# Performance work log

Hardware: AMD Instinct MI355X
Metric: run time of the kernel (lower is better)

Reference implementation:

```python
import jax, jax.numpy as jnp
import numpy as np

DIM = 128
WH, WW = 8, 8
N = WH * WW            # tokens per window = 64
H = 8                  # num_heads
HD = DIM // H          # head_dim = 16
SCALE = HD ** -0.5
B = 2                  # true batch
NW = 1024              # windows per image (256x256 / 8x8)
B_ = B * NW            # 2048 windows total
NFT = 2                # num_frame_type
TABLE = (2 * WH - 1) * (2 * WW - 1)  # 225


def _relative_position_index():
    coords = np.stack(np.meshgrid(np.arange(WH), np.arange(WW), indexing='ij'))  # (2, WH, WW)
    cf = coords.reshape(2, -1)                        # (2, N)
    rel = cf[:, :, None] - cf[:, None, :]             # (2, N, N)
    rel = rel.transpose(1, 2, 0).astype(np.int64)     # (N, N, 2)
    rel[..., 0] += WH - 1
    rel[..., 1] += WW - 1
    rel[..., 0] *= 2 * WW - 1
    return rel.sum(-1)                                # (N, N) in [0, 224]


def setup_inputs() -> dict:
    key = jax.random.key(0)
    ks = jax.random.split(key, 12)
    x = jax.random.normal(ks[0], (B_, N, DIM), dtype=jnp.float32)
    # 0 / -100 additive window mask (shifted-window pattern surrogate)
    mask = jnp.where(jax.random.uniform(ks[1], (NW, N, N)) > 0.9, -100.0, 0.0).astype(jnp.float32)
    frame_type = jax.random.uniform(ks[2], (B, NFT), dtype=jnp.float32)
    qkv_w = jax.random.normal(ks[3], (3 * DIM, DIM), dtype=jnp.float32) * 0.02
    qkv_b = jnp.zeros((3 * DIM,), dtype=jnp.float32)
    table = jax.random.normal(ks[4], (TABLE, H), dtype=jnp.float32) * 0.02
    proj_w = jax.random.normal(ks[5], (DIM, DIM), dtype=jnp.float32) * 0.02
    proj_b = jnp.zeros((DIM,), dtype=jnp.float32)
    aff_w1 = jax.random.normal(ks[6], (16, NFT), dtype=jnp.float32) * 0.1
    aff_b1 = jnp.zeros((16,), dtype=jnp.float32)
    aff_w2 = jax.random.normal(ks[7], (2 * DIM, 16), dtype=jnp.float32) * 0.1
    rel_index = jnp.asarray(_relative_position_index(), dtype=jnp.int32)
    return {"x": x, "mask": mask, "frame_type": frame_type,
            "qkv_w": qkv_w, "qkv_b": qkv_b, "table": table,
            "proj_w": proj_w, "proj_b": proj_b,
            "aff_w1": aff_w1, "aff_b1": aff_b1, "aff_w2": aff_w2,
            "rel_index": rel_index}


def reference(x, mask, frame_type, qkv_w, qkv_b, table, proj_w, proj_b,
              aff_w1, aff_b1, aff_w2, rel_index):
    # qkv projection: (B_, N, 3C) -> (3, B_, H, N, HD)
    qkv = (x @ qkv_w.T + qkv_b).reshape(B_, N, 3, H, HD).transpose(2, 0, 3, 1, 4)
    q, k, v = qkv[0], qkv[1], qkv[2]
    attn = jnp.einsum('bhnd,bhmd->bhnm', q * SCALE, k)          # (B_, H, N, N)
    rpb = table[rel_index].transpose(2, 0, 1)                    # (H, N, N)
    attn = attn + rpb[None]
    # add window mask: (B, NW, H, N, N)
    attn = attn.reshape(B_ // NW, NW, H, N, N) + mask[None, :, None]
    attn = jax.nn.softmax(attn.reshape(B_, H, N, N), axis=-1)
    # FA affine modulation of V
    hdn = jax.nn.sigmoid(frame_type @ aff_w1.T + aff_b1)         # (B, 16)
    ap = hdn @ aff_w2.T                                          # (B, 2C)
    scale_p, bias_p = jnp.split(ap, 2, axis=-1)                  # each (B, C)
    scale_p = jnp.repeat(scale_p, B_ // B, axis=0).reshape(B_, H, 1, HD)
    bias_p = jnp.repeat(bias_p, B_ // B, axis=0).reshape(B_, H, 1, HD)
    v = jax.nn.softplus(scale_p) * v + bias_p
    out = jnp.einsum('bhnm,bhmd->bhnd', attn, v)                 # (B_, H, N, HD)
    out = out.transpose(0, 2, 1, 3).reshape(B_, N, DIM)
    return out @ proj_w.T + proj_b
```

## Files before the change

kernel.cpp:

```cpp
#include <hip/hip_runtime.h>
#include <hip/hip_bf16.h>

#define NWIN 2048
#define LOG2E 1.44269504f
#define QSCALE 0.36067376f

#define OFF_AFF 0
#define OFF_RPB 512
#define OFF_WQ  33280
#define OFF_WP  57856

typedef __attribute__((ext_vector_type(8))) __bf16 bf16x8;
typedef __attribute__((ext_vector_type(4))) float floatx4;
typedef __attribute__((ext_vector_type(4))) short short4v;

#if __has_builtin(__builtin_amdgcn_exp2f)
#define EXP2F __builtin_amdgcn_exp2f
#else
#define EXP2F exp2f
#endif

__global__ __launch_bounds__(256) void prep_kernel(
    const float* __restrict__ frame_type, const float* __restrict__ qkv_w,
    const float* __restrict__ table, const float* __restrict__ proj_w,
    const float* __restrict__ aff_w1, const float* __restrict__ aff_b1,
    const float* __restrict__ aff_w2, const int* __restrict__ rel_index,
    float* __restrict__ ws)
{
  const int gid = blockIdx.x * 256 + threadIdx.x;
  if (gid < 49152) {
    int j = gid & 7, lane = (gid >> 3) & 63, kt = (gid >> 9) & 3, nt = gid >> 11;
    int n = nt * 16 + (lane & 15);
    int k = kt * 32 + (lane >> 4) * 8 + j;
    ((__bf16*)(ws + OFF_WQ))[gid] = (__bf16)qkv_w[n * 128 + k];
  }
  if (gid < 16384) {
    int j = gid & 3, lane = (gid >> 2) & 63, nt = (gid >> 8) & 7, h = gid >> 11;
    int n = nt * 16 + (lane & 15);
    int k = h * 16 + (lane >> 4) * 4 + j;
    ((__bf16*)(ws + OFF_WP))[gid] = (__bf16)proj_w[n * 128 + k];
  }
  if (gid < 32768) {
    int h = gid >> 12, rem = gid & 4095;
    ws[OFF_RPB + gid] = table[rel_index[rem] * 8 + h] * LOG2E;
  }
  if (gid < 512) {
    int b = gid >> 8, c2 = gid & 255;
    float hd[16];
    #pragma unroll
    for (int j = 0; j < 16; ++j) {
      float t = frame_type[b*2+0]*aff_w1[j*2+0] + frame_type[b*2+1]*aff_w1[j*2+1] + aff_b1[j];
      hd[j] = 1.0f / (1.0f + expf(-t));
    }
    float ap = 0.f;
    #pragma unroll
    for (int j = 0; j < 16; ++j) ap += hd[j] * aff_w2[c2*16 + j];
    float r = (c2 < 128) ? ((ap > 20.f) ? ap : log1pf(expf(ap))) : ap;
    ws[OFF_AFF + gid] = r;
  }
}

__global__ __launch_bounds__(256, 3) void attn_kernel(
    const float* __restrict__ x, const float* __restrict__ mask,
    const float* __restrict__ qkv_b, const float* __restrict__ proj_b,
    const float* __restrict__ ws, float* __restrict__ out)
{
  __shared__ __attribute__((aligned(16))) __bf16 sK [64 * 128];
  __shared__ __attribute__((aligned(16))) __bf16 sVT[128 * 64];

#define SKI(row, col) ((row)*128 + ((col) ^ (((row)&7)<<4)))
#define SVI(ch, tok)  ((ch)*64  + ((tok) ^ (((ch)&7)<<3)))

  const int w    = blockIdx.x;
  const int b    = w >> 10;
  const int tid  = threadIdx.x;
  const int wv   = tid >> 6;
  const int lane = tid & 63;
  const int quad = lane >> 4;
  const int l15  = lane & 15;
  const int row0 = wv * 16;

  bf16x8 af[4][4];
  {
    const float* xw = x + (size_t)w * 8192;
    #pragma unroll
    for (int mt = 0; mt < 4; ++mt)
      #pragma unroll
      for (int kt = 0; kt < 4; ++kt) {
        const float* p = xw + (mt*16 + l15) * 128 + kt*32 + quad*8;
        float4 f0 = *(const float4*)p;
        float4 f1 = *(const float4*)(p + 4);
        bf16x8 v;
        v[0]=(__bf16)f0.x; v[1]=(__bf16)f0.y; v[2]=(__bf16)f0.z; v[3]=(__bf16)f0.w;
        v[4]=(__bf16)f1.x; v[5]=(__bf16)f1.y; v[6]=(__bf16)f1.z; v[7]=(__bf16)f1.w;
        af[mt][kt] = v;
      }
  }

  const __bf16* wq = (const __bf16*)(ws + OFF_WQ);

  {
    #pragma unroll
    for (int t = 0; t < 4; ++t) {
      const int nt = 8 + ((t >> 1) << 3) + ((t & 1) << 2) + wv;
      bf16x8 bfr[4];
      #pragma unroll
      for (int kt = 0; kt < 4; ++kt)
        bfr[kt] = *(const bf16x8*)(wq + ((size_t)(nt*4 + kt) * 64 + lane) * 8);
      const float bias = qkv_b[nt*16 + l15];
      const int col = nt*16 + l15;
      #pragma unroll
      for (int mt = 0; mt < 4; ++mt) {
        floatx4 acc = {bias, bias, bias, bias};
        #pragma unroll
        for (int kt = 0; kt < 4; ++kt)
          acc = __builtin_amdgcn_mfma_f32_16x16x32_bf16(af[mt][kt], bfr[kt], acc, 0, 0, 0);
        if (nt < 16) {
          const int c = col - 128;
          const int srow0 = ((((quad & 1) << 1) + (mt >> 1)) << 4)
                          + ((((mt & 1) << 1) | (quad >> 1)) << 2);
          #pragma unroll
          for (int r = 0; r < 4; ++r) sK[SKI(srow0 + r, c)] = (__bf16)acc[r];
        } else {
          const int c = col - 256;
          const float sp = ws[OFF_AFF + b*256 + c];
          const float bp = ws[OFF_AFF + b*256 + 128 + c];
          const int rowb = mt*16 + quad*4;
          #pragma unroll
          for (int r = 0; r < 4; ++r) sVT[SVI(c, rowb + r)] = (__bf16)fmaf(sp, acc[r], bp);
        }
      }
    }
  }

  bf16x8 aq[4];
  #pragma unroll
  for (int kt = 0; kt < 4; ++kt) aq[kt] = af[0][kt];
  #pragma unroll
  for (int mt = 1; mt < 4; ++mt)
    if (wv == mt) {
      #pragma unroll
      for (int kt = 0; kt < 4; ++kt) aq[kt] = af[mt][kt];
    }

  short4v qa[8];
  {
    #pragma unroll
    for (int nt = 0; nt < 8; ++nt) {
      bf16x8 bfr[4];
      #pragma unroll
      for (int kt = 0; kt < 4; ++kt)
        bfr[kt] = *(const bf16x8*)(wq + ((size_t)(nt*4 + kt) * 64 + lane) * 8);
      floatx4 acc = *(const floatx4*)(qkv_b + nt*16 + quad*4);
      #pragma unroll
      for (int kt = 0; kt < 4; ++kt)
        acc = __builtin_amdgcn_mfma_f32_16x16x32_bf16(bfr[kt], aq[kt], acc, 0, 0, 0);
      union { short4v s; __bf16 h4[4]; } u;
      #pragma unroll
      for (int r = 0; r < 4; ++r) u.h4[r] = (__bf16)(acc[r] * QSCALE);
      qa[nt] = u.s;
    }
  }
  __syncthreads();

  floatx4 mv[4];
  {
    const float* mrow = mask + (size_t)(w & 1023) * 4096 + (row0 + l15) * 64;
    #pragma unroll
    for (int jt = 0; jt < 4; ++jt) {
      const int joff = ((jt & 1) << 5) + ((jt >> 1) << 2) + (quad << 3);
      floatx4 m4 = *(const floatx4*)(mrow + joff);
      #pragma unroll
      for (int r = 0; r < 4; ++r) mv[jt][r] = m4[r] * LOG2E;
    }
  }

  floatx4 pacc[8];
  #pragma unroll
  for (int nt = 0; nt < 8; ++nt) {
    float pb = proj_b[nt*16 + l15];
    pacc[nt] = (floatx4){pb, pb, pb, pb};
  }

  bf16x8 ones;
  #pragma unroll
  for (int i = 0; i < 8; ++i) ones[i] = (__bf16)1.0f;

  const float* rpb = ws + OFF_RPB;
  const __bf16* wp = (const __bf16*)(ws + OFF_WP);

  #pragma unroll 1
  for (int h = 0; h < 8; ++h) {
    floatx4 rq[4];
    #pragma unroll
    for (int jt = 0; jt < 4; ++jt) {
      const int joff = ((jt & 1) << 5) + ((jt >> 1) << 2) + (quad << 3);
      rq[jt] = *(const floatx4*)(rpb + h*4096 + (row0 + l15)*64 + joff);
    }
    short4v wpf[8];
    #pragma unroll
    for (int nt = 0; nt < 8; ++nt)
      wpf[nt] = *(const short4v*)(wp + ((size_t)(h*8 + nt)*64 + lane)*4);
    short4v kb[4];
    #pragma unroll
    for (int jt = 0; jt < 4; ++jt)
      kb[jt] = *(const short4v*)(&sK[SKI(jt*16 + l15, h*16 + quad*4)]);

    floatx4 s[4];
    #pragma unroll
    for (int jt = 0; jt < 4; ++jt) {
      floatx4 ci = rq[jt] + mv[jt];
      s[jt] = __builtin_amdgcn_mfma_f32_16x16x16bf16_1k(kb[jt], qa[h], ci, 0, 0, 0);
    }

    union { bf16x8 v; __bf16 e[8]; } p0, p1;
    #pragma unroll
    for (int r = 0; r < 4; ++r) {
      p0.e[r]     = (__bf16)EXP2F(s[0][r]);
      p0.e[4 + r] = (__bf16)EXP2F(s[2][r]);
      p1.e[r]     = (__bf16)EXP2F(s[1][r]);
      p1.e[4 + r] = (__bf16)EXP2F(s[3][r]);
    }

    bf16x8 vb0 = *(const bf16x8*)(&sVT[SVI(h*16 + l15, quad*8)]);
    bf16x8 vb1 = *(const bf16x8*)(&sVT[SVI(h*16 + l15, 32 + quad*8)]);
    floatx4 o2 = {0.f,0.f,0.f,0.f}, sm = {0.f,0.f,0.f,0.f};
    o2 = __builtin_amdgcn_mfma_f32_16x16x32_bf16(vb0, p0.v, o2, 0, 0, 0);
    sm = __builtin_amdgcn_mfma_f32_16x16x32_bf16(ones, p0.v, sm, 0, 0, 0);
    o2 = __builtin_amdgcn_mfma_f32_16x16x32_bf16(vb1, p1.v, o2, 0, 0, 0);
    sm = __builtin_amdgcn_mfma_f32_16x16x32_bf16(ones, p1.v, sm, 0, 0, 0);

    const float inv = 1.0f / sm[0];
    union { short4v s; __bf16 hh[4]; } u;
    #pragma unroll
    for (int r = 0; r < 4; ++r) u.hh[r] = (__bf16)(o2[r] * inv);

    #pragma unroll
    for (int nt = 0; nt < 8; ++nt)
      pacc[nt] = __builtin_amdgcn_mfma_f32_16x16x16bf16_1k(u.s, wpf[nt], pacc[nt], 0, 0, 0);
  }

  {
    float* ow = out + (size_t)w * 8192;
    #pragma unroll
    for (int nt = 0; nt < 8; ++nt)
      #pragma unroll
      for (int r = 0; r < 4; ++r)
        ow[(row0 + quad*4 + r)*128 + nt*16 + l15] = pacc[nt][r];
  }
#undef SKI
#undef SVI
}

extern "C" void kernel_launch(void* const* d_in, const int* in_sizes, int n_in,
                              void* d_out, int out_size, void* d_ws, size_t ws_size,
                              hipStream_t stream)
{
  const float* x          = (const float*)d_in[0];
  const float* mask       = (const float*)d_in[1];
  const float* frame_type = (const float*)d_in[2];
  const float* qkv_w      = (const float*)d_in[3];
  const float* qkv_b      = (const float*)d_in[4];
  const float* table      = (const float*)d_in[5];
  const float* proj_w     = (const float*)d_in[6];
  const float* proj_b     = (const float*)d_in[7];
  const float* aff_w1     = (const float*)d_in[8];
  const float* aff_b1     = (const float*)d_in[9];
  const float* aff_w2     = (const float*)d_in[10];
  const int*   rel_index  = (const int*)d_in[11];
  float* ws   = (float*)d_ws;
  float* outp = (float*)d_out;

  prep_kernel<<<192, 256, 0, stream>>>(frame_type, qkv_w, table, proj_w,
                                       aff_w1, aff_b1, aff_w2, rel_index, ws);
  attn_kernel<<<NWIN, 256, 0, stream>>>(x, mask, qkv_b, proj_b, ws, outp);
}
```

Measured before the change: 226.7 us.

## Process two windows per block sharing mask and weight fragments

Each block now handles window w and window w+1024, which share the same mask, so mask, rpb, QKV and projection weight fragments are loaded once and reused for both. The per-head loop is fully unrolled into a softmax phase followed by a projection phase, and the division is replaced by a hardware reciprocal. The K shared-memory swizzle is also changed. The cost is doubled LDS and register use, which forces occupancy down to 2 blocks per SM, and half as many blocks are launched.

```diff
diff --git a/kernel.cpp b/kernel.cpp
--- a/kernel.cpp
+++ b/kernel.cpp
@@ -1,7 +1,6 @@
 #include <hip/hip_runtime.h>
 #include <hip/hip_bf16.h>
 
-#define NWIN 2048
 #define LOG2E 1.44269504f
 #define QSCALE 0.36067376f
 
@@ -18,6 +17,11 @@
 #define EXP2F __builtin_amdgcn_exp2f
 #else
 #define EXP2F exp2f
+#endif
+#if __has_builtin(__builtin_amdgcn_rcpf)
+#define RCPF __builtin_amdgcn_rcpf
+#else
+#define RCPF(x) (1.0f / (x))
 #endif
 
 __global__ __launch_bounds__(256) void prep_kernel(
@@ -60,19 +64,18 @@
   }
 }
 
-__global__ __launch_bounds__(256, 3) void attn_kernel(
+__global__ __launch_bounds__(256, 2) void attn_kernel(
     const float* __restrict__ x, const float* __restrict__ mask,
     const float* __restrict__ qkv_b, const float* __restrict__ proj_b,
     const float* __restrict__ ws, float* __restrict__ out)
 {
-  __shared__ __attribute__((aligned(16))) __bf16 sK [64 * 128];
-  __shared__ __attribute__((aligned(16))) __bf16 sVT[128 * 64];
-
-#define SKI(row, col) ((row)*128 + ((col) ^ (((row)&7)<<4)))
+  __shared__ __attribute__((aligned(16))) __bf16 sK [2][64 * 128];
+  __shared__ __attribute__((aligned(16))) __bf16 sVT[2][128 * 64];
+
+#define SKI(row, col) ((row)*128 + ((col) ^ (((row)&3)<<4) ^ ((row)&4)))
 #define SVI(ch, tok)  ((ch)*64  + ((tok) ^ (((ch)&7)<<3)))
 
   const int w    = blockIdx.x;
-  const int b    = w >> 10;
   const int tid  = threadIdx.x;
   const int wv   = tid >> 6;
   const int lane = tid & 63;
@@ -80,20 +83,26 @@
   const int l15  = lane & 15;
   const int row0 = wv * 16;
 
-  bf16x8 af[4][4];
-  {
-    const float* xw = x + (size_t)w * 8192;
+  bf16x8 afA[4][4], afB[4][4];
+  {
+    const float* xA = x + (size_t)w * 8192;
+    const float* xB = xA + (size_t)1024 * 8192;
     #pragma unroll
     for (int mt = 0; mt < 4; ++mt)
       #pragma unroll
       for (int kt = 0; kt < 4; ++kt) {
-        const float* p = xw + (mt*16 + l15) * 128 + kt*32 + quad*8;
-        float4 f0 = *(const float4*)p;
-        float4 f1 = *(const float4*)(p + 4);
-        bf16x8 v;
-        v[0]=(__bf16)f0.x; v[1]=(__bf16)f0.y; v[2]=(__bf16)f0.z; v[3]=(__bf16)f0.w;
-        v[4]=(__bf16)f1.x; v[5]=(__bf16)f1.y; v[6]=(__bf16)f1.z; v[7]=(__bf16)f1.w;
-        af[mt][kt] = v;
+        const int off = (mt*16 + l15) * 128 + kt*32 + quad*8;
+        float4 a0 = *(const float4*)(xA + off);
+        float4 a1 = *(const float4*)(xA + off + 4);
+        float4 b0 = *(const float4*)(xB + off);
+        float4 b1 = *(const float4*)(xB + off + 4);
+        bf16x8 va, vb;
+        va[0]=(__bf16)a0.x; va[1]=(__bf16)a0.y; va[2]=(__bf16)a0.z; va[3]=(__bf16)a0.w;
+        va[4]=(__bf16)a1.x; va[5]=(__bf16)a1.y; va[6]=(__bf16)a1.z; va[7]=(__bf16)a1.w;
+        vb[0]=(__bf16)b0.x; vb[1]=(__bf16)b0.y; vb[2]=(__bf16)b0.z; vb[3]=(__bf16)b0.w;
+        vb[4]=(__bf16)b1.x; vb[5]=(__bf16)b1.y; vb[6]=(__bf16)b1.z; vb[7]=(__bf16)b1.w;
+        afA[mt][kt] = va;
+        afB[mt][kt] = vb;
       }
   }
 
@@ -111,39 +120,50 @@
       const int col = nt*16 + l15;
       #pragma unroll
       for (int mt = 0; mt < 4; ++mt) {
-        floatx4 acc = {bias, bias, bias, bias};
+        floatx4 accA = {bias, bias, bias, bias};
+        floatx4 accB = {bias, bias, bias, bias};
         #pragma unroll
-        for (int kt = 0; kt < 4; ++kt)
-          acc = __builtin_amdgcn_mfma_f32_16x16x32_bf16(af[mt][kt], bfr[kt], acc, 0, 0, 0);
+        for (int kt = 0; kt < 4; ++kt) {
+          accA = __builtin_amdgcn_mfma_f32_16x16x32_bf16(afA[mt][kt], bfr[kt], accA, 0, 0, 0);
+          accB = __builtin_amdgcn_mfma_f32_16x16x32_bf16(afB[mt][kt], bfr[kt], accB, 0, 0, 0);
+        }
         if (nt < 16) {
           const int c = col - 128;
           const int srow0 = ((((quad & 1) << 1) + (mt >> 1)) << 4)
                           + ((((mt & 1) << 1) | (quad >> 1)) << 2);
           #pragma unroll
-          for (int r = 0; r < 4; ++r) sK[SKI(srow0 + r, c)] = (__bf16)acc[r];
+          for (int r = 0; r < 4; ++r) {
+            sK[0][SKI(srow0 + r, c)] = (__bf16)accA[r];
+            sK[1][SKI(srow0 + r, c)] = (__bf16)accB[r];
+          }
         } else {
           const int c = col - 256;
-          const float sp = ws[OFF_AFF + b*256 + c];
-          const float bp = ws[OFF_AFF + b*256 + 128 + c];
+          const float spA = ws[OFF_AFF + c];
+          const float bpA = ws[OFF_AFF + 128 + c];
+          const float spB = ws[OFF_AFF + 256 + c];
+          const float bpB = ws[OFF_AFF + 384 + c];
           const int rowb = mt*16 + quad*4;
           #pragma unroll
-          for (int r = 0; r < 4; ++r) sVT[SVI(c, rowb + r)] = (__bf16)fmaf(sp, acc[r], bp);
+          for (int r = 0; r < 4; ++r) {
+            sVT[0][SVI(c, rowb + r)] = (__bf16)fmaf(spA, accA[r], bpA);
+            sVT[1][SVI(c, rowb + r)] = (__bf16)fmaf(spB, accB[r], bpB);
+          }
         }
       }
     }
   }
 
-  bf16x8 aq[4];
+  bf16x8 aqA[4], aqB[4];
   #pragma unroll
-  for (int kt = 0; kt < 4; ++kt) aq[kt] = af[0][kt];
+  for (int kt = 0; kt < 4; ++kt) { aqA[kt] = afA[0][kt]; aqB[kt] = afB[0][kt]; }
   #pragma unroll
   for (int mt = 1; mt < 4; ++mt)
     if (wv == mt) {
       #pragma unroll
-      for (int kt = 0; kt < 4; ++kt) aq[kt] = af[mt][kt];
-    }
-
-  short4v qa[8];
+      for (int kt = 0; kt < 4; ++kt) { aqA[kt] = afA[mt][kt]; aqB[kt] = afB[mt][kt]; }
+    }
+
+  short4v qaA[8], qaB[8];
   {
     #pragma unroll
     for (int nt = 0; nt < 8; ++nt) {
@@ -151,21 +171,28 @@
       #pragma unroll
       for (int kt = 0; kt < 4; ++kt)
         bfr[kt] = *(const bf16x8*)(wq + ((size_t)(nt*4 + kt) * 64 + lane) * 8);
-      floatx4 acc = *(const floatx4*)(qkv_b + nt*16 + quad*4);
-      #pragma unroll
-      for (int kt = 0; kt < 4; ++kt)
-        acc = __builtin_amdgcn_mfma_f32_16x16x32_bf16(bfr[kt], aq[kt], acc, 0, 0, 0);
-      union { short4v s; __bf16 h4[4]; } u;
-      #pragma unroll
-      for (int r = 0; r < 4; ++r) u.h4[r] = (__bf16)(acc[r] * QSCALE);
-      qa[nt] = u.s;
+      floatx4 bias4 = *(const floatx4*)(qkv_b + nt*16 + quad*4);
+      floatx4 accA = bias4, accB = bias4;
+      #pragma unroll
+      for (int kt = 0; kt < 4; ++kt) {
+        accA = __builtin_amdgcn_mfma_f32_16x16x32_bf16(bfr[kt], aqA[kt], accA, 0, 0, 0);
+        accB = __builtin_amdgcn_mfma_f32_16x16x32_bf16(bfr[kt], aqB[kt], accB, 0, 0, 0);
+      }
+      union { short4v s; __bf16 h4[4]; } uA, uB;
+      #pragma unroll
+      for (int r = 0; r < 4; ++r) {
+        uA.h4[r] = (__bf16)(accA[r] * QSCALE);
+        uB.h4[r] = (__bf16)(accB[r] * QSCALE);
+      }
+      qaA[nt] = uA.s;
+      qaB[nt] = uB.s;
     }
   }
   __syncthreads();
 
   floatx4 mv[4];
   {
-    const float* mrow = mask + (size_t)(w & 1023) * 4096 + (row0 + l15) * 64;
+    const float* mrow = mask + (size_t)w * 4096 + (row0 + l15) * 64;
     #pragma unroll
     for (int jt = 0; jt < 4; ++jt) {
       const int joff = ((jt & 1) << 5) + ((jt >> 1) << 2) + (quad << 3);
@@ -175,78 +202,112 @@
     }
   }
 
-  floatx4 pacc[8];
+  bf16x8 ones;
+  #pragma unroll
+  for (int i = 0; i < 8; ++i) ones[i] = (__bf16)1.0f;
+
+  const float* rpb = ws + OFF_RPB;
+  const __bf16* wp = (const __bf16*)(ws + OFF_WP);
+
+#define PHASEA2(H, UA, UB) do {                                              \
+    floatx4 rq_[4];                                                          \
+    short4v kbA_[4], kbB_[4];                                                \
+    _Pragma("unroll")                                                        \
+    for (int jt = 0; jt < 4; ++jt) {                                         \
+      const int joff = ((jt & 1) << 5) + ((jt >> 1) << 2) + (quad << 3);     \
+      rq_[jt] = *(const floatx4*)(rpb + (H)*4096 + (row0 + l15)*64 + joff);  \
+      kbA_[jt] = *(const short4v*)(&sK[0][SKI(jt*16 + l15, (H)*16 + quad*4)]);\
+      kbB_[jt] = *(const short4v*)(&sK[1][SKI(jt*16 + l15, (H)*16 + quad*4)]);\
+    }                                                                        \
+    floatx4 sA_[4], sB_[4];                                                  \
+    _Pragma("unroll")                                                        \
+    for (int jt = 0; jt < 4; ++jt) {                                         \
+      floatx4 ci = rq_[jt] + mv[jt];                                         \
+      sA_[jt] = __builtin_amdgcn_mfma_f32_16x16x16bf16_1k(kbA_[jt], qaA[H], ci, 0, 0, 0); \
+      sB_[jt] = __builtin_amdgcn_mfma_f32_16x16x16bf16_1k(kbB_[jt], qaB[H], ci, 0, 0, 0); \
+    }                                                                        \
+    union { bf16x8 v; __bf16 e[8]; } p0A_, p1A_, p0B_, p1B_;                 \
+    _Pragma("unroll")                                                        \
+    for (int r = 0; r < 4; ++r) {                                            \
+      p0A_.e[r]     = (__bf16)EXP2F(sA_[0][r]);                              \
+      p0A_.e[4 + r] = (__bf16)EXP2F(sA_[2][r]);                              \
+      p1A_.e[r]     = (__bf16)EXP2F(sA_[1][r]);                              \
+      p1A_.e[4 + r] = (__bf16)EXP2F(sA_[3][r]);                              \
+      p0B_.e[r]     = (__bf16)EXP2F(sB_[0][r]);                              \
+      p0B_.e[4 + r] = (__bf16)EXP2F(sB_[2][r]);                              \
+      p1B_.e[r]     = (__bf16)EXP2F(sB_[1][r]);                              \
+      p1B_.e[4 + r] = (__bf16)EXP2F(sB_[3][r]);                              \
+    }                                                                        \
+    bf16x8 vbA0 = *(const bf16x8*)(&sVT[0][SVI((H)*16 + l15, quad*8)]);      \
+    bf16x8 vbA1 = *(const bf16x8*)(&sVT[0][SVI((H)*16 + l15, 32 + quad*8)]); \
+    bf16x8 vbB0 = *(const bf16x8*)(&sVT[1][SVI((H)*16 + l15, quad*8)]);      \
+    bf16x8 vbB1 = *(const bf16x8*)(&sVT[1][SVI((H)*16 + l15, 32 + quad*8)]); \
+    floatx4 o2A = {0.f,0.f,0.f,0.f}, smA = {0.f,0.f,0.f,0.f};                \
+    floatx4 o2B = {0.f,0.f,0.f,0.f}, smB = {0.f,0.f,0.f,0.f};                \
+    o2A = __builtin_amdgcn_mfma_f32_16x16x32_bf16(vbA0, p0A_.v, o2A, 0, 0, 0);\
+    o2B = __builtin_amdgcn_mfma_f32_16x16x32_bf16(vbB0, p0B_.v, o2B, 0, 0, 0);\
+    smA = __builtin_amdgcn_mfma_f32_16x16x32_bf16(ones, p0A_.v, smA, 0, 0, 0);\
+    smB = __builtin_amdgcn_mfma_f32_16x16x32_bf16(ones, p0B_.v, smB, 0, 0, 0);\
+    o2A = __builtin_amdgcn_mfma_f32_16x16x32_bf16(vbA1, p1A_.v, o2A, 0, 0, 0);\
+    o2B = __builtin_amdgcn_mfma_f32_16x16x32_bf16(vbB1, p1B_.v, o2B, 0, 0, 0);\
+    smA = __builtin_amdgcn_mfma_f32_16x16x32_bf16(ones, p1A_.v, smA, 0, 0, 0);\
+    smB = __builtin_amdgcn_mfma_f32_16x16x32_bf16(ones, p1B_.v, smB, 0, 0, 0);\
+    const float invA = RCPF(smA[0]);                                         \
+    const float invB = RCPF(smB[0]);                                         \
+    union { short4v s; __bf16 hh_[4]; } uA_, uB_;                            \
+    _Pragma("unroll")                                                        \
+    for (int r = 0; r < 4; ++r) {                                            \
+      uA_.hh_[r] = (__bf16)(o2A[r] * invA);                                  \
+      uB_.hh_[r] = (__bf16)(o2B[r] * invB);                                  \
+    }                                                                        \
+    UA = uA_.s; UB = uB_.s;                                                  \
+  } while (0)
+
+  short4v uA0, uA1, uA2, uA3, uA4, uA5, uA6, uA7;
+  short4v uB0, uB1, uB2, uB3, uB4, uB5, uB6, uB7;
+  PHASEA2(0, uA0, uB0); PHASEA2(1, uA1, uB1);
+  PHASEA2(2, uA2, uB2); PHASEA2(3, uA3, uB3);
+  PHASEA2(4, uA4, uB4); PHASEA2(5, uA5, uB5);
+  PHASEA2(6, uA6, uB6); PHASEA2(7, uA7, uB7);
+#undef PHASEA2
+
+  floatx4 paccA[8], paccB[8];
   #pragma unroll
   for (int nt = 0; nt < 8; ++nt) {
     float pb = proj_b[nt*16 + l15];
-    pacc[nt] = (floatx4){pb, pb, pb, pb};
-  }
-
-  bf16x8 ones;
-  #pragma unroll
-  for (int i = 0; i < 8; ++i) ones[i] = (__bf16)1.0f;
-
-  const float* rpb = ws + OFF_RPB;
-  const __bf16* wp = (const __bf16*)(ws + OFF_WP);
-
-  #pragma unroll 1
-  for (int h = 0; h < 8; ++h) {
-    floatx4 rq[4];
-    #pragma unroll
-    for (int jt = 0; jt < 4; ++jt) {
-      const int joff = ((jt & 1) << 5) + ((jt >> 1) << 2) + (quad << 3);
-      rq[jt] = *(const floatx4*)(rpb + h*4096 + (row0 + l15)*64 + joff);
-    }
-    short4v wpf[8];
+    paccA[nt] = (floatx4){pb, pb, pb, pb};
+    paccB[nt] = (floatx4){pb, pb, pb, pb};
+  }
+
+#define PHASEB2(H, UA, UB) do {                                              \
+    short4v wpf_[8];                                                         \
+    _Pragma("unroll")                                                        \
+    for (int nt = 0; nt < 8; ++nt)                                           \
+      wpf_[nt] = *(const short4v*)(wp + ((size_t)((H)*8 + nt)*64 + lane)*4); \
+    _Pragma("unroll")                                                        \
+    for (int nt = 0; nt < 8; ++nt) {                                         \
+      paccA[nt] = __builtin_amdgcn_mfma_f32_16x16x16bf16_1k(UA, wpf_[nt], paccA[nt], 0, 0, 0); \
+      paccB[nt] = __builtin_amdgcn_mfma_f32_16x16x16bf16_1k(UB, wpf_[nt], paccB[nt], 0, 0, 0); \
+    }                                                                        \
+  } while (0)
+
+  PHASEB2(0, uA0, uB0); PHASEB2(1, uA1, uB1);
+  PHASEB2(2, uA2, uB2); PHASEB2(3, uA3, uB3);
+  PHASEB2(4, uA4, uB4); PHASEB2(5, uA5, uB5);
+  PHASEB2(6, uA6, uB6); PHASEB2(7, uA7, uB7);
+#undef PHASEB2
+
+  {
+    float* owA = out + (size_t)w * 8192;
+    float* owB = owA + (size_t)1024 * 8192;
     #pragma unroll
     for (int nt = 0; nt < 8; ++nt)
-      wpf[nt] = *(const short4v*)(wp + ((size_t)(h*8 + nt)*64 + lane)*4);
-    short4v kb[4];
-    #pragma unroll
-    for (int jt = 0; jt < 4; ++jt)
-      kb[jt] = *(const short4v*)(&sK[SKI(jt*16 + l15, h*16 + quad*4)]);
-
-    floatx4 s[4];
-    #pragma unroll
-    for (int jt = 0; jt < 4; ++jt) {
-      floatx4 ci = rq[jt] + mv[jt];
-      s[jt] = __builtin_amdgcn_mfma_f32_16x16x16bf16_1k(kb[jt], qa[h], ci, 0, 0, 0);
-    }
-
-    union { bf16x8 v; __bf16 e[8]; } p0, p1;
-    #pragma unroll
-    for (int r = 0; r < 4; ++r) {
-      p0.e[r]     = (__bf16)EXP2F(s[0][r]);
-      p0.e[4 + r] = (__bf16)EXP2F(s[2][r]);
-      p1.e[r]     = (__bf16)EXP2F(s[1][r]);
-      p1.e[4 + r] = (__bf16)EXP2F(s[3][r]);
-    }
-
-    bf16x8 vb0 = *(const bf16x8*)(&sVT[SVI(h*16 + l15, quad*8)]);
-    bf16x8 vb1 = *(const bf16x8*)(&sVT[SVI(h*16 + l15, 32 + quad*8)]);
-    floatx4 o2 = {0.f,0.f,0.f,0.f}, sm = {0.f,0.f,0.f,0.f};
-    o2 = __builtin_amdgcn_mfma_f32_16x16x32_bf16(vb0, p0.v, o2, 0, 0, 0);
-    sm = __builtin_amdgcn_mfma_f32_16x16x32_bf16(ones, p0.v, sm, 0, 0, 0);
-    o2 = __builtin_amdgcn_mfma_f32_16x16x32_bf16(vb1, p1.v, o2, 0, 0, 0);
-    sm = __builtin_amdgcn_mfma_f32_16x16x32_bf16(ones, p1.v, sm, 0, 0, 0);
-
-    const float inv = 1.0f / sm[0];
-    union { short4v s; __bf16 hh[4]; } u;
-    #pragma unroll
-    for (int r = 0; r < 4; ++r) u.hh[r] = (__bf16)(o2[r] * inv);
-
-    #pragma unroll
-    for (int nt = 0; nt < 8; ++nt)
-      pacc[nt] = __builtin_amdgcn_mfma_f32_16x16x16bf16_1k(u.s, wpf[nt], pacc[nt], 0, 0, 0);
-  }
-
-  {
-    float* ow = out + (size_t)w * 8192;
-    #pragma unroll
-    for (int nt = 0; nt < 8; ++nt)
-      #pragma unroll
-      for (int r = 0; r < 4; ++r)
-        ow[(row0 + quad*4 + r)*128 + nt*16 + l15] = pacc[nt][r];
+      #pragma unroll
+      for (int r = 0; r < 4; ++r) {
+        const int off = (row0 + quad*4 + r)*128 + nt*16 + l15;
+        owA[off] = paccA[nt][r];
+        owB[off] = paccB[nt][r];
+      }
   }
 #undef SKI
 #undef SVI
@@ -273,5 +334,5 @@
 
   prep_kernel<<<192, 256, 0, stream>>>(frame_type, qkv_w, table, proj_w,
                                        aff_w1, aff_b1, aff_w2, rel_index, ws);
-  attn_kernel<<<NWIN, 256, 0, stream>>>(x, mask, qkv_b, proj_b, ws, outp);
+  attn_kernel<<<1024, 256, 0, stream>>>(x, mask, qkv_b, proj_b, ws, outp);
 }
```

After: 203.9 us. 1.11x faster.
